# Optimization experiments

Measured on AMD Instinct MI355X. Metric: run time of the kernel, lower is better.

Reference implementation:

```python
import jax, jax.numpy as jnp
import numpy as np

B, D = 256, 8                 # trees, tree depth (leaves at level D)
V, E, H = 32000, 128, 128     # vocab, embedding_dim, hidden_dim
N = 2 ** (D + 1) - 1          # 511 heap-indexed nodes per tree


def setup_inputs() -> dict:
    key = jax.random.key(0)
    ks = jax.random.split(key, 9)
    s = 0.05  # keep gate pre-activations in a sane range
    return {
        "tokens": jax.random.randint(ks[0], (B, N), 0, V),
        "arity": jax.random.randint(ks[1], (B, 2 ** D - 1), 0, 2).astype(jnp.int32),
        "emb": jax.random.normal(ks[2], (V, E), dtype=jnp.float32) * s,
        "W": jax.random.normal(ks[3], (4, E, H), dtype=jnp.float32) * s,      # i,f,o,u
        "bW": jax.random.normal(ks[4], (4, H), dtype=jnp.float32) * s,
        "Ubin": jax.random.normal(ks[5], (5, 2 * H, H), dtype=jnp.float32) * s,  # i,f_l,f_r,o,u
        "bUbin": jax.random.normal(ks[6], (5, H), dtype=jnp.float32) * s,
        "Uun": jax.random.normal(ks[7], (4, H, H), dtype=jnp.float32) * s,    # i,f,o,u
        "bUun": jax.random.normal(ks[8], (4, H), dtype=jnp.float32) * s,
    }


def reference(tokens, arity, emb, W, bW, Ubin, bUbin, Uun, bUun):
    # Level-synchronous bottom-up Tree-LSTM over heap-indexed perfect trees.
    x = emb[tokens]  # [B, N, E] embedding gather for every node
    depth = int(np.log2(tokens.shape[1] + 1)) - 1

    # Leaves (level `depth`): h = tanh(W_u x + b_u), c = 0
    off = 2 ** depth - 1
    lx = x[:, off:]  # [B, 2^D, E]
    h = jnp.tanh(jnp.einsum('bne,eh->bnh', lx, W[3]) + bW[3])
    c = jnp.zeros_like(h)

    for l in range(depth - 1, -1, -1):
        o2, cnt = 2 ** l - 1, 2 ** l
        nx = x[:, o2:o2 + cnt]            # [B, cnt, E] this level's tokens
        h_l, h_r = h[:, ::2], h[:, 1::2]   # children (heap order)
        c_l, c_r = c[:, ::2], c[:, 1::2]

        # Shared input projections for all 4 gates, fused into one GEMM
        Wx = jnp.einsum('bne,geh->gbnh', nx, W) + bW[:, None, None, :]
        hcat = jnp.concatenate([h_l, h_r], axis=-1)  # [B, cnt, 2H]
        Ub = jnp.einsum('bnk,gkh->gbnh', hcat, Ubin) + bUbin[:, None, None, :]
        Uu = jnp.einsum('bnh,gha->gbna', h_l, Uun) + bUun[:, None, None, :]

        # Binary branch: i, f_l, f_r (shared W_f), o, u
        i_b = jax.nn.sigmoid(Wx[0] + Ub[0])
        f_lg = jax.nn.sigmoid(Wx[1] + Ub[1])
        f_rg = jax.nn.sigmoid(Wx[1] + Ub[2])
        o_b = jax.nn.sigmoid(Wx[2] + Ub[3])
        u_b = jnp.tanh(Wx[3] + Ub[4])
        c_b = i_b * u_b + f_lg * c_l + f_rg * c_r
        h_b = o_b * jnp.tanh(c_b)

        # Unary branch (child = left child)
        i_u = jax.nn.sigmoid(Wx[0] + Uu[0])
        f_u = jax.nn.sigmoid(Wx[1] + Uu[1])
        o_u = jax.nn.sigmoid(Wx[2] + Uu[2])
        u_u = jnp.tanh(Wx[3] + Uu[3])
        c_u = i_u * u_u + f_u * c_l
        h_u = o_u * jnp.tanh(c_u)

        m = (arity[:, o2:o2 + cnt] == 1)[..., None]  # True -> binary node
        h = jnp.where(m, h_b, h_u)
        c = jnp.where(m, c_b, c_u)

    return h[:, 0], c[:, 0]  # root (h, c), each [B, H]
```

## Files before the change

### kernel.cpp

```cpp
#include <hip/hip_runtime.h>
#include <hip/hip_bf16.h>

#define NTOK 511
#define NINT 255

typedef unsigned short u16;
typedef __attribute__((ext_vector_type(8))) short bf16x8;
typedef __attribute__((ext_vector_type(4))) float f32x4;

constexpr int OFF_FLAG = 0;
constexpr int OFF_WB   = 4;
constexpr int W3B = 294912;
constexpr int WB_ELEMS = 311296;
constexpr int OFF_BIAS = OFF_WB + WB_ELEMS / 2;
constexpr int BW4 = 0, BUB4 = 512, BUB1 = 1024, BUU4 = 1152, B3 = 1664;
constexpr int BIAS_FLOATS = 1792;
constexpr int OFF_ROOT  = OFF_BIAS + BIAS_FLOATS;
constexpr int OFF_CHUNK = OFF_ROOT + 65536;
constexpr long PER_TREE = 49152;

__device__ __forceinline__ float bf2f(__hip_bfloat16 v) { return __bfloat162float(v); }
__device__ __forceinline__ short f2s(float f) {
    __hip_bfloat16 b = __float2bfloat16(f);
    return *reinterpret_cast<short*>(&b);
}
__device__ __forceinline__ float sigm(float x) { return 1.0f / (1.0f + __expf(-x)); }
__device__ __forceinline__ float tanh_(float x) { return 1.0f - 2.0f / (__expf(2.0f * x) + 1.0f); }

__device__ __forceinline__ float ldf(const void* p, long idx, int isbf) {
    return isbf ? bf2f(((const __hip_bfloat16*)p)[idx]) : ((const float*)p)[idx];
}

__device__ __forceinline__ bf16x8 ldA(const void* p, long idx, int isbf) {
    if (isbf) return *(const bf16x8*)((const short*)p + idx);
    const float* f = (const float*)p + idx;
    float4 a = *(const float4*)f, b = *(const float4*)(f + 4);
    bf16x8 r;
    r[0] = f2s(a.x); r[1] = f2s(a.y); r[2] = f2s(a.z); r[3] = f2s(a.w);
    r[4] = f2s(b.x); r[5] = f2s(b.y); r[6] = f2s(b.z); r[7] = f2s(b.w);
    return r;
}

typedef const __attribute__((address_space(1))) unsigned int* gp1_t;
typedef __attribute__((address_space(3))) unsigned int* lp3_t;
__device__ __forceinline__ void stage16(const void* g, void* l) {
    __builtin_amdgcn_global_load_lds((gp1_t)g, (lp3_t)l, 16, 0, 0);
}

__global__ void detect_kernel(const void* W, float* ws) {
    if (threadIdx.x == 0 && blockIdx.x == 0) {
        const u16* u = (const u16*)W;
        int cnt = 0;
        for (int i = 0; i < 128; i += 2) {
            u16 x = u[i];
            int ex = (x >> 7) & 0xff;
            if (x == 0 || (ex >= 96 && ex <= 127)) cnt++;
        }
        ((int*)ws)[0] = (cnt >= 48) ? 1 : 0;
    }
}

__global__ __launch_bounds__(256) void repack_mfma(
    const void* W, const void* bW, const void* Ubin, const void* bUbin,
    const void* Uun, const void* bUun, float* ws)
{
    const int isbf = ((const int*)ws)[0];
    short* wb = (short*)(ws + OFF_WB);
    float* bias = ws + OFF_BIAS;
    int tid = blockIdx.x * blockDim.x + threadIdx.x;
    int nth = gridDim.x * blockDim.x;

    for (int idx = tid; idx < 294912; idx += nth) {
        int e = idx & 511, fjc = idx >> 9;
        int jc = fjc / 72, f = fjc - jc * 72;
        int lane = e >> 3, id8 = e & 7;
        int j = jc * 16 + (lane & 15);
        float v;
        if (f < 16) {
            int g = f >> 2, ks = f & 3;
            int k = ks * 32 + (lane >> 4) * 8 + id8;
            v = ldf(W, (long)g * 16384 + k * 128 + j, isbf);
        } else if (f < 32) {
            int fu = f - 16; int g = fu >> 2, ks = fu & 3;
            int k = ks * 32 + (lane >> 4) * 8 + id8;
            v = ldf(Uun, (long)g * 16384 + k * 128 + j, isbf);
        } else {
            int fb = f - 32; int g = fb >> 3, ks = fb & 7;
            int k = ks * 32 + (lane >> 4) * 8 + id8;
            v = ldf(Ubin, (long)g * 32768 + k * 128 + j, isbf);
        }
        wb[idx] = f2s(v);
    }
    for (int idx = tid; idx < 16384; idx += nth) {
        int e = idx & 511, frag = idx >> 9;
        int jc = frag >> 2, ks = frag & 3;
        int lane = e >> 3, id8 = e & 7;
        int k = ks * 32 + (lane >> 4) * 8 + id8;
        int j = jc * 16 + (lane & 15);
        wb[W3B + idx] = f2s(ldf(W, (long)3 * 16384 + k * 128 + j, isbf));
    }
    for (int j = tid; j < 128; j += nth) {
        float4 b;
        b.x = ldf(bW, 0 * 128 + j, isbf); b.y = ldf(bW, 1 * 128 + j, isbf);
        b.z = ldf(bW, 2 * 128 + j, isbf); b.w = ldf(bW, 3 * 128 + j, isbf);
        ((float4*)(bias + BW4))[j] = b;
        float4 bb;
        bb.x = ldf(bUbin, 0 * 128 + j, isbf); bb.y = ldf(bUbin, 1 * 128 + j, isbf);
        bb.z = ldf(bUbin, 2 * 128 + j, isbf); bb.w = ldf(bUbin, 3 * 128 + j, isbf);
        ((float4*)(bias + BUB4))[j] = bb;
        (bias + BUB1)[j] = ldf(bUbin, 4 * 128 + j, isbf);
        float4 bu;
        bu.x = ldf(bUun, 0 * 128 + j, isbf); bu.y = ldf(bUun, 1 * 128 + j, isbf);
        bu.z = ldf(bUun, 2 * 128 + j, isbf); bu.w = ldf(bUun, 3 * 128 + j, isbf);
        ((float4*)(bias + BUU4))[j] = bu;
        (bias + B3)[j] = ldf(bW, 3 * 128 + j, isbf);
    }
}

#define MFMA(A, B, C) __builtin_amdgcn_mfma_f32_16x16x32_bf16(A, B, C, 0, 0, 0)

__global__ __launch_bounds__(256, 2) void leaf_mfma(
    const int* __restrict__ tokens, const void* emb, const float* __restrict__ ws,
    short* __restrict__ hOut, int treeOff, int Mtot, int iters)
{
    __shared__ short hst[4][16][132];
    const int t = threadIdx.x;
    const int isbf = ((const int*)ws)[0];
    const int wv = t >> 6, lane = t & 63, quad = lane >> 4, l16 = lane & 15;
    const short* wb = (const short*)(ws + OFF_WB);
    const float* bias = ws + OFF_BIAS;

    bf16x8 bf[32];
#pragma unroll
    for (int f = 0; f < 32; ++f)
        bf[f] = *(const bf16x8*)(wb + W3B + f * 512 + lane * 8);
    float b3v[8];
#pragma unroll
    for (int jc = 0; jc < 8; ++jc) b3v[jc] = (bias + B3)[jc * 16 + l16];

    for (int it = 0; it < iters; ++it) {
        int rb = (blockIdx.x * iters + it) * 64 + wv * 16;
        if (rb >= Mtot) break;
        int p = rb + l16; if (p >= Mtot) p = Mtot - 1;
        int bl = p >> 8, i = p & 255;
        int tk = tokens[(long)(treeOff + bl) * NTOK + 255 + i];
        bf16x8 ax[4];
#pragma unroll
        for (int ks = 0; ks < 4; ++ks)
            ax[ks] = ldA(emb, (long)tk * 128 + ks * 32 + quad * 8, isbf);
        f32x4 acc[8];
#pragma unroll
        for (int jc = 0; jc < 8; ++jc) acc[jc] = {0.f, 0.f, 0.f, 0.f};
#pragma unroll
        for (int jc = 0; jc < 8; ++jc)
#pragma unroll
            for (int ks = 0; ks < 4; ++ks)
                acc[jc] = MFMA(ax[ks], bf[jc * 4 + ks], acc[jc]);
#pragma unroll
        for (int jc = 0; jc < 8; ++jc)
#pragma unroll
            for (int r = 0; r < 4; ++r)
                hst[wv][quad * 4 + r][jc * 16 + l16] = f2s(tanh_(acc[jc][r] + b3v[jc]));
        int nloc = lane >> 2, c0 = (lane & 3) * 4;
        int prow = rb + nloc;
        if (prow < Mtot) {
#pragma unroll
            for (int jcb = 0; jcb < 8; ++jcb) {
                uint2 v = *(const uint2*)&hst[wv][nloc][jcb * 16 + c0];
                *(uint2*)&hOut[((long)jcb * Mtot + prow) * 16 + c0] = v;
            }
        }
    }
}

__global__ __launch_bounds__(256, 2) void level2_mfma(
    const int* __restrict__ tokens, const int* __restrict__ arity, const void* emb,
    const float* __restrict__ ws, const short* __restrict__ hChild,
    const float* __restrict__ cChild, short* __restrict__ hOut, float* __restrict__ cOut,
    int lvl, int treeOff, int leafchild, int Mtot, int Mchild,
    int NBMB, int Q)
{
    __shared__ short Bs[72 * 512];
    __shared__ short hst[4][16][20];

    const int t = threadIdx.x;
    const int isbf = ((const int*)ws)[0];
    const int jc = blockIdx.x / NBMB;
    const int mb = blockIdx.x - jc * NBMB;
    const int wv = t >> 6, lane = t & 63, quad = lane >> 4, l16 = lane & 15;
    const int cnt = 1 << lvl, o2 = cnt - 1;
    const short* wb = (const short*)(ws + OFF_WB);
    const float* bias = ws + OFF_BIAS;
    const short* wj = wb + (long)jc * 36864;

#pragma unroll
    for (int s = 0; s < 18; ++s) {
        int off = (s * 256 + t) * 8;
        stage16(wj + off, Bs + off);
    }

    const int j = jc * 16 + l16;
    const float4 bw = ((const float4*)(bias + BW4))[j];
    const float4 bb = ((const float4*)(bias + BUB4))[j];
    const float  b1 = (bias + BUB1)[j];
    const float4 bu = ((const float4*)(bias + BUU4))[j];

    __syncthreads();

    for (int q = 0; q < Q; ++q) {
        const int p0 = (mb * Q + q) * 64;
        if (p0 >= Mtot) break;

        int row = wv * 16 + l16;
        int p = p0 + row; if (p >= Mtot) p = Mtot - 1;
        int bl = p >> lvl, i = p - (bl << lvl);
        long crow = (long)bl * (cnt << 1) + 2 * i;
        int tk = tokens[(long)(treeOff + bl) * NTOK + o2 + i];
        bf16x8 ax[4], ah[8];
#pragma unroll
        for (int ks = 0; ks < 4; ++ks)
            ax[ks] = ldA(emb, (long)tk * 128 + ks * 32 + quad * 8, isbf);
#pragma unroll
        for (int ks = 0; ks < 8; ++ks) {
            int k0 = ks * 32 + quad * 8;
            int side = k0 >> 7, kl = k0 & 127;
            ah[ks] = *(const bf16x8*)(hChild +
                ((long)(kl >> 4) * Mchild + crow + side) * 16 + (kl & 15));
        }

        f32x4 aW[4], aU[4], aB[5];
#pragma unroll
        for (int g = 0; g < 4; ++g) { aW[g] = {0,0,0,0}; aU[g] = {0,0,0,0}; }
#pragma unroll
        for (int g = 0; g < 5; ++g) aB[g] = {0,0,0,0};

#pragma unroll
        for (int f = 0; f < 16; ++f) {
            bf16x8 b = *(const bf16x8*)&Bs[f * 512 + lane * 8];
            aW[f >> 2] = MFMA(ax[f & 3], b, aW[f >> 2]);
        }
#pragma unroll
        for (int f = 16; f < 32; ++f) {
            bf16x8 b = *(const bf16x8*)&Bs[f * 512 + lane * 8];
            aU[(f - 16) >> 2] = MFMA(ah[(f - 16) & 3], b, aU[(f - 16) >> 2]);
        }
#pragma unroll
        for (int f = 32; f < 72; ++f) {
            bf16x8 b = *(const bf16x8*)&Bs[f * 512 + lane * 8];
            int fb = f - 32;
            aB[fb >> 3] = MFMA(ah[fb & 7], b, aB[fb >> 3]);
        }

        int arv[4]; float clv[4], crv[4];
#pragma unroll
        for (int r = 0; r < 4; ++r) {
            int pe = p0 + wv * 16 + quad * 4 + r;
            if (pe >= Mtot) pe = Mtot - 1;
            int ble = pe >> lvl, ie = pe - (ble << lvl);
            arv[r] = arity[(long)(treeOff + ble) * NINT + o2 + ie];
            if (!leafchild) {
                long crowe = (long)ble * (cnt << 1) + 2 * ie;
                clv[r] = cChild[((long)jc * Mchild + crowe) * 16 + l16];
                crv[r] = cChild[((long)jc * Mchild + crowe + 1) * 16 + l16];
            } else { clv[r] = 0.f; crv[r] = 0.f; }
        }

#pragma unroll
        for (int r = 0; r < 4; ++r) {
            int ml = wv * 16 + quad * 4 + r;
            int pr = p0 + ml;
            bool val = (pr < Mtot);
            int pc = val ? pr : Mtot - 1;
            bool bin = (arv[r] == 1);
            float w0 = aW[0][r] + bw.x;
            float w1 = aW[1][r] + bw.y;
            float w2 = aW[2][r] + bw.z;
            float w3 = aW[3][r] + bw.w;
            float pi, pf, po, pu;
            if (bin) { pi = w0 + aB[0][r] + bb.x; pf = w1 + aB[1][r] + bb.y;
                       po = w2 + aB[3][r] + bb.w; pu = w3 + aB[4][r] + b1; }
            else     { pi = w0 + aU[0][r] + bu.x; pf = w1 + aU[1][r] + bu.y;
                       po = w2 + aU[2][r] + bu.z; pu = w3 + aU[3][r] + bu.w; }
            float cl = clv[r];
            float cr = bin ? crv[r] : 0.f;
            float frv = bin ? sigm(w1 + aB[2][r] + bb.z) : 0.f;
            float ig = sigm(pi), fg = sigm(pf), og = sigm(po), ug = tanh_(pu);
            float c = ig * ug + fg * cl + frv * cr;
            float h = og * tanh_(c);
            if (val) cOut[((long)jc * Mtot + pc) * 16 + l16] = c;
            hst[wv][quad * 4 + r][l16] = f2s(h);
        }
        {
            int nloc = lane >> 2, c0 = (lane & 3) * 4;
            int prow = p0 + wv * 16 + nloc;
            if (prow < Mtot) {
                uint2 v = *(const uint2*)&hst[wv][nloc][c0];
                *(uint2*)&hOut[((long)jc * Mtot + prow) * 16 + c0] = v;
            }
        }
    }
}

__global__ __launch_bounds__(256, 2) void level_direct(
    const int* __restrict__ tokens, const int* __restrict__ arity, const void* emb,
    const float* __restrict__ ws, const short* __restrict__ hChild,
    const float* __restrict__ cChild, short* __restrict__ hOut, float* __restrict__ cOut,
    float* __restrict__ rootH, float* __restrict__ rootC,
    int lvl, int treeOff, int isRoot, int Mtot, int Mchild, int NBM)
{
    __shared__ short hst[4][16][20];

    const int t = threadIdx.x;
    const int isbf = ((const int*)ws)[0];
    const int jc = blockIdx.x / NBM;
    const int mb = blockIdx.x - jc * NBM;
    const int wv = t >> 6, lane = t & 63, quad = lane >> 4, l16 = lane & 15;
    const int cnt = 1 << lvl, o2 = cnt - 1;
    const short* wb = (const short*)(ws + OFF_WB);
    const float* bias = ws + OFF_BIAS;
    const short* wj = wb + (long)jc * 36864;

    const int j = jc * 16 + l16;
    const float4 bw = ((const float4*)(bias + BW4))[j];
    const float4 bb = ((const float4*)(bias + BUB4))[j];
    const float  b1 = (bias + BUB1)[j];
    const float4 bu = ((const float4*)(bias + BUU4))[j];

    const int p0 = mb * 64;

    int row = wv * 16 + l16;
    int p = p0 + row; if (p >= Mtot) p = Mtot - 1;
    int bl = p >> lvl, i = p - (bl << lvl);
    long crow = (long)bl * (cnt << 1) + 2 * i;
    int tk = tokens[(long)(treeOff + bl) * NTOK + o2 + i];
    bf16x8 ax[4], ah[8];
#pragma unroll
    for (int ks = 0; ks < 4; ++ks)
        ax[ks] = ldA(emb, (long)tk * 128 + ks * 32 + quad * 8, isbf);
#pragma unroll
    for (int ks = 0; ks < 8; ++ks) {
        int k0 = ks * 32 + quad * 8;
        int side = k0 >> 7, kl = k0 & 127;
        ah[ks] = *(const bf16x8*)(hChild +
            ((long)(kl >> 4) * Mchild + crow + side) * 16 + (kl & 15));
    }

    f32x4 aW[4], aU[4], aB[5];
#pragma unroll
    for (int g = 0; g < 4; ++g) { aW[g] = {0,0,0,0}; aU[g] = {0,0,0,0}; }
#pragma unroll
    for (int g = 0; g < 5; ++g) aB[g] = {0,0,0,0};

#pragma unroll
    for (int f = 0; f < 16; ++f) {
        bf16x8 b = *(const bf16x8*)(wj + f * 512 + lane * 8);
        aW[f >> 2] = MFMA(ax[f & 3], b, aW[f >> 2]);
    }
#pragma unroll
    for (int f = 16; f < 32; ++f) {
        bf16x8 b = *(const bf16x8*)(wj + f * 512 + lane * 8);
        aU[(f - 16) >> 2] = MFMA(ah[(f - 16) & 3], b, aU[(f - 16) >> 2]);
    }
#pragma unroll
    for (int f = 32; f < 72; ++f) {
        bf16x8 b = *(const bf16x8*)(wj + f * 512 + lane * 8);
        int fb = f - 32;
        aB[fb >> 3] = MFMA(ah[fb & 7], b, aB[fb >> 3]);
    }

    int arv[4]; float clv[4], crv[4];
#pragma unroll
    for (int r = 0; r < 4; ++r) {
        int pe = p0 + wv * 16 + quad * 4 + r;
        if (pe >= Mtot) pe = Mtot - 1;
        int ble = pe >> lvl, ie = pe - (ble << lvl);
        arv[r] = arity[(long)(treeOff + ble) * NINT + o2 + ie];
        long crowe = (long)ble * (cnt << 1) + 2 * ie;
        clv[r] = cChild[((long)jc * Mchild + crowe) * 16 + l16];
        crv[r] = cChild[((long)jc * Mchild + crowe + 1) * 16 + l16];
    }

#pragma unroll
    for (int r = 0; r < 4; ++r) {
        int ml = wv * 16 + quad * 4 + r;
        int pr = p0 + ml;
        bool val = (pr < Mtot);
        int pc = val ? pr : Mtot - 1;
        int ble = pc >> lvl;
        bool bin = (arv[r] == 1);
        float w0 = aW[0][r] + bw.x;
        float w1 = aW[1][r] + bw.y;
        float w2 = aW[2][r] + bw.z;
        float w3 = aW[3][r] + bw.w;
        float pi, pf, po, pu;
        if (bin) { pi = w0 + aB[0][r] + bb.x; pf = w1 + aB[1][r] + bb.y;
                   po = w2 + aB[3][r] + bb.w; pu = w3 + aB[4][r] + b1; }
        else     { pi = w0 + aU[0][r] + bu.x; pf = w1 + aU[1][r] + bu.y;
                   po = w2 + aU[2][r] + bu.z; pu = w3 + aU[3][r] + bu.w; }
        float cl = clv[r];
        float cr = bin ? crv[r] : 0.f;
        float frv = bin ? sigm(w1 + aB[2][r] + bb.z) : 0.f;
        float ig = sigm(pi), fg = sigm(pf), og = sigm(po), ug = tanh_(pu);
        float c = ig * ug + fg * cl + frv * cr;
        float h = og * tanh_(c);
        if (isRoot) {
            if (val) {
                rootH[(long)(treeOff + ble) * 128 + j] = h;
                rootC[(long)(treeOff + ble) * 128 + j] = c;
            }
        } else {
            if (val) cOut[((long)jc * Mtot + pc) * 16 + l16] = c;
            hst[wv][quad * 4 + r][l16] = f2s(h);
        }
    }
    if (!isRoot) {
        int nloc = lane >> 2, c0 = (lane & 3) * 4;
        int prow = p0 + wv * 16 + nloc;
        if (prow < Mtot) {
            uint2 v = *(const uint2*)&hst[wv][nloc][c0];
            *(uint2*)&hOut[((long)jc * Mtot + prow) * 16 + c0] = v;
        }
    }
}

__global__ __launch_bounds__(256) void out_kernel(const float* ws, void* out)
{
    const int isbf = ((const int*)ws)[0];
    const float* rootH = ws + OFF_ROOT;
    const float* rootC = rootH + 32768;
    int t = blockIdx.x * 256 + threadIdx.x;
    float h = rootH[t], c = rootC[t];
    if (isbf) {
        ((__hip_bfloat16*)out)[t]         = __float2bfloat16(h);
        ((__hip_bfloat16*)out)[32768 + t] = __float2bfloat16(c);
    } else {
        ((float*)out)[t]         = h;
        ((float*)out)[32768 + t] = c;
    }
}

extern "C" void kernel_launch(void* const* d_in, const int* in_sizes, int n_in,
                              void* d_out, int out_size, void* d_ws, size_t ws_size,
                              hipStream_t stream)
{
    const int* tokens = (const int*)d_in[0];
    const int* arity  = (const int*)d_in[1];
    const void* emb   = d_in[2];
    const void* W     = d_in[3];
    const void* bW    = d_in[4];
    const void* Ubin  = d_in[5];
    const void* bUbin = d_in[6];
    const void* Uun   = d_in[7];
    const void* bUun  = d_in[8];

    float* ws = (float*)d_ws;

    int Bc = 256;
    while (Bc > 1 && (size_t)(OFF_CHUNK + Bc * PER_TREE) * 4 > ws_size) Bc >>= 1;
    const int nCh = 256 / Bc;

    detect_kernel<<<1, 64, 0, stream>>>(W, ws);
    repack_mfma<<<128, 256, 0, stream>>>(W, bW, Ubin, bUbin, Uun, bUun, ws);

    short* Ha = (short*)(ws + OFF_CHUNK);
    short* Hb = Ha + (long)Bc * 32768;
    float* Ca = (float*)(Hb + (long)Bc * 16384);
    float* Cb = Ca + (long)Bc * 8192;
    float* rootH = ws + OFF_ROOT;
    float* rootC = rootH + 32768;

    for (int cidx = 0; cidx < nCh; ++cidx) {
        int toff = cidx * Bc;
        {
            int Mleaf = Bc * 256;
            int NBL = (Mleaf + 63) / 64; if (NBL > 512) NBL = 512;
            int itersL = (Mleaf + NBL * 64 - 1) / (NBL * 64);
            leaf_mfma<<<NBL, 256, 0, stream>>>(tokens, emb, ws, Ha, toff, Mleaf, itersL);
        }
        for (int l = 7; l >= 5; --l) {
            int M = Bc << l;
            int Mchild = Bc << (l + 1);
            const short* hC = (l & 1) ? Ha : Hb;
            const float* cC = (l & 1) ? Ca : Cb;
            short* hO = (l & 1) ? Hb : Ha;
            float* cO = (l & 1) ? Cb : Ca;
            int lc = (l == 7) ? 1 : 0;
            int NBM = (M + 63) / 64;
            int Q = (NBM + 127) / 128;
            int NBMB = (NBM + Q - 1) / Q;
            level2_mfma<<<dim3(NBMB * 8), 256, 0, stream>>>(
                tokens, arity, emb, ws, hC, cC, hO, cO,
                l, toff, lc, M, Mchild, NBMB, Q);
        }
        for (int l = 4; l >= 0; --l) {
            int M = Bc << l;
            int Mchild = Bc << (l + 1);
            const short* hC = (l & 1) ? Ha : Hb;
            const float* cC = (l & 1) ? Ca : Cb;
            short* hO = (l & 1) ? Hb : Ha;
            float* cO = (l & 1) ? Cb : Ca;
            int isRoot = (l == 0) ? 1 : 0;
            int NBM = (M + 63) / 64;
            level_direct<<<dim3(NBM * 8), 256, 0, stream>>>(
                tokens, arity, emb, ws, hC, cC, hO, cO, rootH, rootC,
                l, toff, isRoot, M, Mchild, NBM);
        }
    }
    out_kernel<<<128, 256, 0, stream>>>(ws, d_out);
}
```

Before: 184.4 us.

## Process two M-tiles per wave in level2_mfma to reuse LDS weight fragments

level2_mfma becomes a template over MT row tiles per wave, so each B fragment read from LDS feeds MT MFMAs. The host now launches MT=2 with 128 nodes per block and half the grid. The child c-state loads are hoisted ahead of the MFMA chain and the arity loads moved into the epilogue, in both level2_mfma and level_direct, to overlap memory latency with compute. This raises register pressure (double the accumulators and A fragments) and halves block-level parallelism.

Measured after the change: 182.5 us. About the same (-1.0%).

```diff
diff --git a/kernel.cpp b/kernel.cpp
--- a/kernel.cpp
+++ b/kernel.cpp
@@ -173,6 +173,7 @@
     }
 }
 
+template <int MT>
 __global__ __launch_bounds__(256, 2) void level2_mfma(
     const int* __restrict__ tokens, const int* __restrict__ arity, const void* emb,
     const float* __restrict__ ws, const short* __restrict__ hChild,
@@ -181,8 +182,9 @@
     int NBMB, int Q)
 {
     __shared__ short Bs[72 * 512];
-    __shared__ short hst[4][16][20];
-
+    __shared__ short hst[4][MT][16][20];
+
+    constexpr int NODES = 64 * MT;
     const int t = threadIdx.x;
     const int isbf = ((const int*)ws)[0];
     const int jc = blockIdx.x / NBMB;
@@ -208,94 +210,117 @@
     __syncthreads();
 
     for (int q = 0; q < Q; ++q) {
-        const int p0 = (mb * Q + q) * 64;
+        const int p0 = (mb * Q + q) * NODES;
         if (p0 >= Mtot) break;
 
-        int row = wv * 16 + l16;
-        int p = p0 + row; if (p >= Mtot) p = Mtot - 1;
-        int bl = p >> lvl, i = p - (bl << lvl);
-        long crow = (long)bl * (cnt << 1) + 2 * i;
-        int tk = tokens[(long)(treeOff + bl) * NTOK + o2 + i];
-        bf16x8 ax[4], ah[8];
-#pragma unroll
-        for (int ks = 0; ks < 4; ++ks)
-            ax[ks] = ldA(emb, (long)tk * 128 + ks * 32 + quad * 8, isbf);
-#pragma unroll
-        for (int ks = 0; ks < 8; ++ks) {
-            int k0 = ks * 32 + quad * 8;
-            int side = k0 >> 7, kl = k0 & 127;
-            ah[ks] = *(const bf16x8*)(hChild +
-                ((long)(kl >> 4) * Mchild + crow + side) * 16 + (kl & 15));
-        }
-
-        f32x4 aW[4], aU[4], aB[5];
-#pragma unroll
-        for (int g = 0; g < 4; ++g) { aW[g] = {0,0,0,0}; aU[g] = {0,0,0,0}; }
-#pragma unroll
-        for (int g = 0; g < 5; ++g) aB[g] = {0,0,0,0};
+        bf16x8 ax[MT][4], ah[MT][8];
+#pragma unroll
+        for (int mt = 0; mt < MT; ++mt) {
+            int row = wv * (16 * MT) + mt * 16 + l16;
+            int p = p0 + row; if (p >= Mtot) p = Mtot - 1;
+            int bl = p >> lvl, i = p - (bl << lvl);
+            long crow = (long)bl * (cnt << 1) + 2 * i;
+            int tk = tokens[(long)(treeOff + bl) * NTOK + o2 + i];
+#pragma unroll
+            for (int ks = 0; ks < 4; ++ks)
+                ax[mt][ks] = ldA(emb, (long)tk * 128 + ks * 32 + quad * 8, isbf);
+#pragma unroll
+            for (int ks = 0; ks < 8; ++ks) {
+                int k0 = ks * 32 + quad * 8;
+                int side = k0 >> 7, kl = k0 & 127;
+                ah[mt][ks] = *(const bf16x8*)(hChild +
+                    ((long)(kl >> 4) * Mchild + crow + side) * 16 + (kl & 15));
+            }
+        }
+
+        float clv[MT][4], crv[MT][4];
+#pragma unroll
+        for (int mt = 0; mt < MT; ++mt)
+#pragma unroll
+        for (int r = 0; r < 4; ++r) {
+            if (!leafchild) {
+                int pe = p0 + wv * (16 * MT) + mt * 16 + quad * 4 + r;
+                if (pe >= Mtot) pe = Mtot - 1;
+                int ble = pe >> lvl, ie = pe - (ble << lvl);
+                long crowe = (long)ble * (cnt << 1) + 2 * ie;
+                clv[mt][r] = cChild[((long)jc * Mchild + crowe) * 16 + l16];
+                crv[mt][r] = cChild[((long)jc * Mchild + crowe + 1) * 16 + l16];
+            } else { clv[mt][r] = 0.f; crv[mt][r] = 0.f; }
+        }
+
+        f32x4 aW[4][MT], aU[4][MT], aB[5][MT];
+#pragma unroll
+        for (int g = 0; g < 4; ++g)
+#pragma unroll
+            for (int mt = 0; mt < MT; ++mt) { aW[g][mt] = {0,0,0,0}; aU[g][mt] = {0,0,0,0}; }
+#pragma unroll
+        for (int g = 0; g < 5; ++g)
+#pragma unroll
+            for (int mt = 0; mt < MT; ++mt) aB[g][mt] = {0,0,0,0};
 
 #pragma unroll
         for (int f = 0; f < 16; ++f) {
             bf16x8 b = *(const bf16x8*)&Bs[f * 512 + lane * 8];
-            aW[f >> 2] = MFMA(ax[f & 3], b, aW[f >> 2]);
+#pragma unroll
+            for (int mt = 0; mt < MT; ++mt)
+                aW[f >> 2][mt] = MFMA(ax[mt][f & 3], b, aW[f >> 2][mt]);
         }
 #pragma unroll
         for (int f = 16; f < 32; ++f) {
             bf16x8 b = *(const bf16x8*)&Bs[f * 512 + lane * 8];
-            aU[(f - 16) >> 2] = MFMA(ah[(f - 16) & 3], b, aU[(f - 16) >> 2]);
+            int g = (f - 16) >> 2, ks = (f - 16) & 3;
+#pragma unroll
+            for (int mt = 0; mt < MT; ++mt)
+                aU[g][mt] = MFMA(ah[mt][ks], b, aU[g][mt]);
         }
 #pragma unroll
         for (int f = 32; f < 72; ++f) {
             bf16x8 b = *(const bf16x8*)&Bs[f * 512 + lane * 8];
-            int fb = f - 32;
-            aB[fb >> 3] = MFMA(ah[fb & 7], b, aB[fb >> 3]);
-        }
-
-        int arv[4]; float clv[4], crv[4];
-#pragma unroll
-        for (int r = 0; r < 4; ++r) {
-            int pe = p0 + wv * 16 + quad * 4 + r;
-            if (pe >= Mtot) pe = Mtot - 1;
-            int ble = pe >> lvl, ie = pe - (ble << lvl);
-            arv[r] = arity[(long)(treeOff + ble) * NINT + o2 + ie];
-            if (!leafchild) {
-                long crowe = (long)ble * (cnt << 1) + 2 * ie;
-                clv[r] = cChild[((long)jc * Mchild + crowe) * 16 + l16];
-                crv[r] = cChild[((long)jc * Mchild + crowe + 1) * 16 + l16];
-            } else { clv[r] = 0.f; crv[r] = 0.f; }
-        }
-
-#pragma unroll
-        for (int r = 0; r < 4; ++r) {
-            int ml = wv * 16 + quad * 4 + r;
-            int pr = p0 + ml;
-            bool val = (pr < Mtot);
-            int pc = val ? pr : Mtot - 1;
-            bool bin = (arv[r] == 1);
-            float w0 = aW[0][r] + bw.x;
-            float w1 = aW[1][r] + bw.y;
-            float w2 = aW[2][r] + bw.z;
-            float w3 = aW[3][r] + bw.w;
-            float pi, pf, po, pu;
-            if (bin) { pi = w0 + aB[0][r] + bb.x; pf = w1 + aB[1][r] + bb.y;
-                       po = w2 + aB[3][r] + bb.w; pu = w3 + aB[4][r] + b1; }
-            else     { pi = w0 + aU[0][r] + bu.x; pf = w1 + aU[1][r] + bu.y;
-                       po = w2 + aU[2][r] + bu.z; pu = w3 + aU[3][r] + bu.w; }
-            float cl = clv[r];
-            float cr = bin ? crv[r] : 0.f;
-            float frv = bin ? sigm(w1 + aB[2][r] + bb.z) : 0.f;
-            float ig = sigm(pi), fg = sigm(pf), og = sigm(po), ug = tanh_(pu);
-            float c = ig * ug + fg * cl + frv * cr;
-            float h = og * tanh_(c);
-            if (val) cOut[((long)jc * Mtot + pc) * 16 + l16] = c;
-            hst[wv][quad * 4 + r][l16] = f2s(h);
+            int fb = f - 32, g = fb >> 3, ks = fb & 7;
+#pragma unroll
+            for (int mt = 0; mt < MT; ++mt)
+                aB[g][mt] = MFMA(ah[mt][ks], b, aB[g][mt]);
+        }
+
+#pragma unroll
+        for (int mt = 0; mt < MT; ++mt) {
+#pragma unroll
+            for (int r = 0; r < 4; ++r) {
+                int ml = wv * (16 * MT) + mt * 16 + quad * 4 + r;
+                int pr = p0 + ml;
+                bool val = (pr < Mtot);
+                int pc = val ? pr : Mtot - 1;
+                int ble = pc >> lvl, ie = pc - (ble << lvl);
+                int arvv = arity[(long)(treeOff + ble) * NINT + o2 + ie];
+                bool bin = (arvv == 1);
+                float w0 = aW[0][mt][r] + bw.x;
+                float w1 = aW[1][mt][r] + bw.y;
+                float w2 = aW[2][mt][r] + bw.z;
+                float w3 = aW[3][mt][r] + bw.w;
+                float pi, pf, po, pu;
+                if (bin) { pi = w0 + aB[0][mt][r] + bb.x; pf = w1 + aB[1][mt][r] + bb.y;
+                           po = w2 + aB[3][mt][r] + bb.w; pu = w3 + aB[4][mt][r] + b1; }
+                else     { pi = w0 + aU[0][mt][r] + bu.x; pf = w1 + aU[1][mt][r] + bu.y;
+                           po = w2 + aU[2][mt][r] + bu.z; pu = w3 + aU[3][mt][r] + bu.w; }
+                float cl = clv[mt][r];
+                float cr = bin ? crv[mt][r] : 0.f;
+                float frv = bin ? sigm(w1 + aB[2][mt][r] + bb.z) : 0.f;
+                float ig = sigm(pi), fg = sigm(pf), og = sigm(po), ug = tanh_(pu);
+                float c = ig * ug + fg * cl + frv * cr;
+                float h = og * tanh_(c);
+                if (val) cOut[((long)jc * Mtot + pc) * 16 + l16] = c;
+                hst[wv][mt][quad * 4 + r][l16] = f2s(h);
+            }
         }
         {
             int nloc = lane >> 2, c0 = (lane & 3) * 4;
-            int prow = p0 + wv * 16 + nloc;
-            if (prow < Mtot) {
-                uint2 v = *(const uint2*)&hst[wv][nloc][c0];
-                *(uint2*)&hOut[((long)jc * Mtot + prow) * 16 + c0] = v;
+#pragma unroll
+            for (int mt = 0; mt < MT; ++mt) {
+                int prow = p0 + wv * (16 * MT) + mt * 16 + nloc;
+                if (prow < Mtot) {
+                    uint2 v = *(const uint2*)&hst[wv][mt][nloc][c0];
+                    *(uint2*)&hOut[((long)jc * Mtot + prow) * 16 + c0] = v;
+                }
             }
         }
     }
@@ -345,6 +370,17 @@
             ((long)(kl >> 4) * Mchild + crow + side) * 16 + (kl & 15));
     }
 
+    float clv[4], crv[4];
+#pragma unroll
+    for (int r = 0; r < 4; ++r) {
+        int pe = p0 + wv * 16 + quad * 4 + r;
+        if (pe >= Mtot) pe = Mtot - 1;
+        int ble = pe >> lvl, ie = pe - (ble << lvl);
+        long crowe = (long)ble * (cnt << 1) + 2 * ie;
+        clv[r] = cChild[((long)jc * Mchild + crowe) * 16 + l16];
+        crv[r] = cChild[((long)jc * Mchild + crowe + 1) * 16 + l16];
+    }
+
     f32x4 aW[4], aU[4], aB[5];
 #pragma unroll
     for (int g = 0; g < 4; ++g) { aW[g] = {0,0,0,0}; aU[g] = {0,0,0,0}; }
@@ -366,18 +402,6 @@
         bf16x8 b = *(const bf16x8*)(wj + f * 512 + lane * 8);
         int fb = f - 32;
         aB[fb >> 3] = MFMA(ah[fb & 7], b, aB[fb >> 3]);
-    }
-
-    int arv[4]; float clv[4], crv[4];
-#pragma unroll
-    for (int r = 0; r < 4; ++r) {
-        int pe = p0 + wv * 16 + quad * 4 + r;
-        if (pe >= Mtot) pe = Mtot - 1;
-        int ble = pe >> lvl, ie = pe - (ble << lvl);
-        arv[r] = arity[(long)(treeOff + ble) * NINT + o2 + ie];
-        long crowe = (long)ble * (cnt << 1) + 2 * ie;
-        clv[r] = cChild[((long)jc * Mchild + crowe) * 16 + l16];
-        crv[r] = cChild[((long)jc * Mchild + crowe + 1) * 16 + l16];
     }
 
 #pragma unroll
@@ -386,8 +410,9 @@
         int pr = p0 + ml;
         bool val = (pr < Mtot);
         int pc = val ? pr : Mtot - 1;
-        int ble = pc >> lvl;
-        bool bin = (arv[r] == 1);
+        int ble = pc >> lvl, ie = pc - (ble << lvl);
+        int arvv = arity[(long)(treeOff + ble) * NINT + o2 + ie];
+        bool bin = (arvv == 1);
         float w0 = aW[0][r] + bw.x;
         float w1 = aW[1][r] + bw.y;
         float w2 = aW[2][r] + bw.z;
@@ -485,10 +510,10 @@
             short* hO = (l & 1) ? Hb : Ha;
             float* cO = (l & 1) ? Cb : Ca;
             int lc = (l == 7) ? 1 : 0;
-            int NBM = (M + 63) / 64;
-            int Q = (NBM + 127) / 128;
+            int NBM = (M + 127) / 128;
+            int Q = (NBM + 63) / 64;
             int NBMB = (NBM + Q - 1) / Q;
-            level2_mfma<<<dim3(NBMB * 8), 256, 0, stream>>>(
+            level2_mfma<2><<<dim3(NBMB * 8), 256, 0, stream>>>(
                 tokens, arity, emb, ws, hC, cC, hO, cO,
                 l, toff, lc, M, Mchild, NBMB, Q);
         }
```

## Unify level kernels into one direct-load kernel with grouped block swizzle

Applied to the files above, without the earlier changes.

Replaces the LDS-staged level2_mfma kernel (used for levels 7..5) and level_direct with a single level_all kernel. It reads weight fragments straight from global memory instead of staging 72 KB into shared memory, and raises the occupancy hint to 3 blocks per SM. When NBM is a multiple of 8, it remaps block IDs so neighbouring blocks share row tiles across the 8 column chunks, which should improve L2 reuse of activations. The aim is to cut LDS staging and the per-block sync and to run more blocks at once, at the cost of heavier global/L2 traffic for weights and losing the multi-tile Q loop that amortised staging.

New measurement: 233.5 us. +26.6%, slower.

```diff
diff --git a/kernel.cpp b/kernel.cpp
--- a/kernel.cpp
+++ b/kernel.cpp
@@ -39,12 +39,6 @@
     r[0] = f2s(a.x); r[1] = f2s(a.y); r[2] = f2s(a.z); r[3] = f2s(a.w);
     r[4] = f2s(b.x); r[5] = f2s(b.y); r[6] = f2s(b.z); r[7] = f2s(b.w);
     return r;
-}
-
-typedef const __attribute__((address_space(1))) unsigned int* gp1_t;
-typedef __attribute__((address_space(3))) unsigned int* lp3_t;
-__device__ __forceinline__ void stage16(const void* g, void* l) {
-    __builtin_amdgcn_global_load_lds((gp1_t)g, (lp3_t)l, 16, 0, 0);
 }
 
 __global__ void detect_kernel(const void* W, float* ws) {
@@ -173,159 +167,33 @@
     }
 }
 
-__global__ __launch_bounds__(256, 2) void level2_mfma(
+__global__ __launch_bounds__(256, 3) void level_all(
     const int* __restrict__ tokens, const int* __restrict__ arity, const void* emb,
     const float* __restrict__ ws, const short* __restrict__ hChild,
     const float* __restrict__ cChild, short* __restrict__ hOut, float* __restrict__ cOut,
-    int lvl, int treeOff, int leafchild, int Mtot, int Mchild,
-    int NBMB, int Q)
-{
-    __shared__ short Bs[72 * 512];
+    float* __restrict__ rootH, float* __restrict__ rootC,
+    int lvl, int treeOff, int leafchild, int isRoot, int Mtot, int Mchild, int NBM)
+{
     __shared__ short hst[4][16][20];
 
     const int t = threadIdx.x;
     const int isbf = ((const int*)ws)[0];
-    const int jc = blockIdx.x / NBMB;
-    const int mb = blockIdx.x - jc * NBMB;
+    int jc, mb;
+    {
+        int bid = blockIdx.x;
+        if ((NBM & 7) == 0) {
+            int g = bid >> 6, r = bid & 63;
+            jc = r >> 3; mb = g * 8 + (r & 7);
+        } else {
+            jc = bid / NBM; mb = bid - jc * NBM;
+        }
+    }
     const int wv = t >> 6, lane = t & 63, quad = lane >> 4, l16 = lane & 15;
     const int cnt = 1 << lvl, o2 = cnt - 1;
     const short* wb = (const short*)(ws + OFF_WB);
     const float* bias = ws + OFF_BIAS;
     const short* wj = wb + (long)jc * 36864;
-
-#pragma unroll
-    for (int s = 0; s < 18; ++s) {
-        int off = (s * 256 + t) * 8;
-        stage16(wj + off, Bs + off);
-    }
-
     const int j = jc * 16 + l16;
-    const float4 bw = ((const float4*)(bias + BW4))[j];
-    const float4 bb = ((const float4*)(bias + BUB4))[j];
-    const float  b1 = (bias + BUB1)[j];
-    const float4 bu = ((const float4*)(bias + BUU4))[j];
-
-    __syncthreads();
-
-    for (int q = 0; q < Q; ++q) {
-        const int p0 = (mb * Q + q) * 64;
-        if (p0 >= Mtot) break;
-
-        int row = wv * 16 + l16;
-        int p = p0 + row; if (p >= Mtot) p = Mtot - 1;
-        int bl = p >> lvl, i = p - (bl << lvl);
-        long crow = (long)bl * (cnt << 1) + 2 * i;
-        int tk = tokens[(long)(treeOff + bl) * NTOK + o2 + i];
-        bf16x8 ax[4], ah[8];
-#pragma unroll
-        for (int ks = 0; ks < 4; ++ks)
-            ax[ks] = ldA(emb, (long)tk * 128 + ks * 32 + quad * 8, isbf);
-#pragma unroll
-        for (int ks = 0; ks < 8; ++ks) {
-            int k0 = ks * 32 + quad * 8;
-            int side = k0 >> 7, kl = k0 & 127;
-            ah[ks] = *(const bf16x8*)(hChild +
-                ((long)(kl >> 4) * Mchild + crow + side) * 16 + (kl & 15));
-        }
-
-        f32x4 aW[4], aU[4], aB[5];
-#pragma unroll
-        for (int g = 0; g < 4; ++g) { aW[g] = {0,0,0,0}; aU[g] = {0,0,0,0}; }
-#pragma unroll
-        for (int g = 0; g < 5; ++g) aB[g] = {0,0,0,0};
-
-#pragma unroll
-        for (int f = 0; f < 16; ++f) {
-            bf16x8 b = *(const bf16x8*)&Bs[f * 512 + lane * 8];
-            aW[f >> 2] = MFMA(ax[f & 3], b, aW[f >> 2]);
-        }
-#pragma unroll
-        for (int f = 16; f < 32; ++f) {
-            bf16x8 b = *(const bf16x8*)&Bs[f * 512 + lane * 8];
-            aU[(f - 16) >> 2] = MFMA(ah[(f - 16) & 3], b, aU[(f - 16) >> 2]);
-        }
-#pragma unroll
-        for (int f = 32; f < 72; ++f) {
-            bf16x8 b = *(const bf16x8*)&Bs[f * 512 + lane * 8];
-            int fb = f - 32;
-            aB[fb >> 3] = MFMA(ah[fb & 7], b, aB[fb >> 3]);
-        }
-
-        int arv[4]; float clv[4], crv[4];
-#pragma unroll
-        for (int r = 0; r < 4; ++r) {
-            int pe = p0 + wv * 16 + quad * 4 + r;
-            if (pe >= Mtot) pe = Mtot - 1;
-            int ble = pe >> lvl, ie = pe - (ble << lvl);
-            arv[r] = arity[(long)(treeOff + ble) * NINT + o2 + ie];
-            if (!leafchild) {
-                long crowe = (long)ble * (cnt << 1) + 2 * ie;
-                clv[r] = cChild[((long)jc * Mchild + crowe) * 16 + l16];
-                crv[r] = cChild[((long)jc * Mchild + crowe + 1) * 16 + l16];
-            } else { clv[r] = 0.f; crv[r] = 0.f; }
-        }
-
-#pragma unroll
-        for (int r = 0; r < 4; ++r) {
-            int ml = wv * 16 + quad * 4 + r;
-            int pr = p0 + ml;
-            bool val = (pr < Mtot);
-            int pc = val ? pr : Mtot - 1;
-            bool bin = (arv[r] == 1);
-            float w0 = aW[0][r] + bw.x;
-            float w1 = aW[1][r] + bw.y;
-            float w2 = aW[2][r] + bw.z;
-            float w3 = aW[3][r] + bw.w;
-            float pi, pf, po, pu;
-            if (bin) { pi = w0 + aB[0][r] + bb.x; pf = w1 + aB[1][r] + bb.y;
-                       po = w2 + aB[3][r] + bb.w; pu = w3 + aB[4][r] + b1; }
-            else     { pi = w0 + aU[0][r] + bu.x; pf = w1 + aU[1][r] + bu.y;
-                       po = w2 + aU[2][r] + bu.z; pu = w3 + aU[3][r] + bu.w; }
-            float cl = clv[r];
-            float cr = bin ? crv[r] : 0.f;
-            float frv = bin ? sigm(w1 + aB[2][r] + bb.z) : 0.f;
-            float ig = sigm(pi), fg = sigm(pf), og = sigm(po), ug = tanh_(pu);
-            float c = ig * ug + fg * cl + frv * cr;
-            float h = og * tanh_(c);
-            if (val) cOut[((long)jc * Mtot + pc) * 16 + l16] = c;
-            hst[wv][quad * 4 + r][l16] = f2s(h);
-        }
-        {
-            int nloc = lane >> 2, c0 = (lane & 3) * 4;
-            int prow = p0 + wv * 16 + nloc;
-            if (prow < Mtot) {
-                uint2 v = *(const uint2*)&hst[wv][nloc][c0];
-                *(uint2*)&hOut[((long)jc * Mtot + prow) * 16 + c0] = v;
-            }
-        }
-    }
-}
-
-__global__ __launch_bounds__(256, 2) void level_direct(
-    const int* __restrict__ tokens, const int* __restrict__ arity, const void* emb,
-    const float* __restrict__ ws, const short* __restrict__ hChild,
-    const float* __restrict__ cChild, short* __restrict__ hOut, float* __restrict__ cOut,
-    float* __restrict__ rootH, float* __restrict__ rootC,
-    int lvl, int treeOff, int isRoot, int Mtot, int Mchild, int NBM)
-{
-    __shared__ short hst[4][16][20];
-
-    const int t = threadIdx.x;
-    const int isbf = ((const int*)ws)[0];
-    const int jc = blockIdx.x / NBM;
-    const int mb = blockIdx.x - jc * NBM;
-    const int wv = t >> 6, lane = t & 63, quad = lane >> 4, l16 = lane & 15;
-    const int cnt = 1 << lvl, o2 = cnt - 1;
-    const short* wb = (const short*)(ws + OFF_WB);
-    const float* bias = ws + OFF_BIAS;
-    const short* wj = wb + (long)jc * 36864;
-
-    const int j = jc * 16 + l16;
-    const float4 bw = ((const float4*)(bias + BW4))[j];
-    const float4 bb = ((const float4*)(bias + BUB4))[j];
-    const float  b1 = (bias + BUB1)[j];
-    const float4 bu = ((const float4*)(bias + BUU4))[j];
-
     const int p0 = mb * 64;
 
     int row = wv * 16 + l16;
@@ -345,29 +213,6 @@
             ((long)(kl >> 4) * Mchild + crow + side) * 16 + (kl & 15));
     }
 
-    f32x4 aW[4], aU[4], aB[5];
-#pragma unroll
-    for (int g = 0; g < 4; ++g) { aW[g] = {0,0,0,0}; aU[g] = {0,0,0,0}; }
-#pragma unroll
-    for (int g = 0; g < 5; ++g) aB[g] = {0,0,0,0};
-
-#pragma unroll
-    for (int f = 0; f < 16; ++f) {
-        bf16x8 b = *(const bf16x8*)(wj + f * 512 + lane * 8);
-        aW[f >> 2] = MFMA(ax[f & 3], b, aW[f >> 2]);
-    }
-#pragma unroll
-    for (int f = 16; f < 32; ++f) {
-        bf16x8 b = *(const bf16x8*)(wj + f * 512 + lane * 8);
-        aU[(f - 16) >> 2] = MFMA(ah[(f - 16) & 3], b, aU[(f - 16) >> 2]);
-    }
-#pragma unroll
-    for (int f = 32; f < 72; ++f) {
-        bf16x8 b = *(const bf16x8*)(wj + f * 512 + lane * 8);
-        int fb = f - 32;
-        aB[fb >> 3] = MFMA(ah[fb & 7], b, aB[fb >> 3]);
-    }
-
     int arv[4]; float clv[4], crv[4];
 #pragma unroll
     for (int r = 0; r < 4; ++r) {
@@ -375,10 +220,40 @@
         if (pe >= Mtot) pe = Mtot - 1;
         int ble = pe >> lvl, ie = pe - (ble << lvl);
         arv[r] = arity[(long)(treeOff + ble) * NINT + o2 + ie];
-        long crowe = (long)ble * (cnt << 1) + 2 * ie;
-        clv[r] = cChild[((long)jc * Mchild + crowe) * 16 + l16];
-        crv[r] = cChild[((long)jc * Mchild + crowe + 1) * 16 + l16];
-    }
+        if (!leafchild) {
+            long crowe = (long)ble * (cnt << 1) + 2 * ie;
+            clv[r] = cChild[((long)jc * Mchild + crowe) * 16 + l16];
+            crv[r] = cChild[((long)jc * Mchild + crowe + 1) * 16 + l16];
+        } else { clv[r] = 0.f; crv[r] = 0.f; }
+    }
+
+    f32x4 aW[4], aU[4], aB[5];
+#pragma unroll
+    for (int g = 0; g < 4; ++g) { aW[g] = {0,0,0,0}; aU[g] = {0,0,0,0}; }
+#pragma unroll
+    for (int g = 0; g < 5; ++g) aB[g] = {0,0,0,0};
+
+#pragma unroll
+    for (int f = 0; f < 16; ++f) {
+        bf16x8 b = *(const bf16x8*)(wj + f * 512 + lane * 8);
+        aW[f >> 2] = MFMA(ax[f & 3], b, aW[f >> 2]);
+    }
+#pragma unroll
+    for (int f = 16; f < 32; ++f) {
+        bf16x8 b = *(const bf16x8*)(wj + f * 512 + lane * 8);
+        aU[(f - 16) >> 2] = MFMA(ah[(f - 16) & 3], b, aU[(f - 16) >> 2]);
+    }
+#pragma unroll
+    for (int f = 32; f < 72; ++f) {
+        bf16x8 b = *(const bf16x8*)(wj + f * 512 + lane * 8);
+        int fb = f - 32;
+        aB[fb >> 3] = MFMA(ah[fb & 7], b, aB[fb >> 3]);
+    }
+
+    const float4 bw = ((const float4*)(bias + BW4))[j];
+    const float4 bb = ((const float4*)(bias + BUB4))[j];
+    const float  b1 = (bias + BUB1)[j];
+    const float4 bu = ((const float4*)(bias + BUU4))[j];
 
 #pragma unroll
     for (int r = 0; r < 4; ++r) {
@@ -477,7 +352,7 @@
             int itersL = (Mleaf + NBL * 64 - 1) / (NBL * 64);
             leaf_mfma<<<NBL, 256, 0, stream>>>(tokens, emb, ws, Ha, toff, Mleaf, itersL);
         }
-        for (int l = 7; l >= 5; --l) {
+        for (int l = 7; l >= 0; --l) {
             int M = Bc << l;
             int Mchild = Bc << (l + 1);
             const short* hC = (l & 1) ? Ha : Hb;
@@ -485,25 +360,11 @@
             short* hO = (l & 1) ? Hb : Ha;
             float* cO = (l & 1) ? Cb : Ca;
             int lc = (l == 7) ? 1 : 0;
-            int NBM = (M + 63) / 64;
-            int Q = (NBM + 127) / 128;
-            int NBMB = (NBM + Q - 1) / Q;
-            level2_mfma<<<dim3(NBMB * 8), 256, 0, stream>>>(
-                tokens, arity, emb, ws, hC, cC, hO, cO,
-                l, toff, lc, M, Mchild, NBMB, Q);
-        }
-        for (int l = 4; l >= 0; --l) {
-            int M = Bc << l;
-            int Mchild = Bc << (l + 1);
-            const short* hC = (l & 1) ? Ha : Hb;
-            const float* cC = (l & 1) ? Ca : Cb;
-            short* hO = (l & 1) ? Hb : Ha;
-            float* cO = (l & 1) ? Cb : Ca;
             int isRoot = (l == 0) ? 1 : 0;
             int NBM = (M + 63) / 64;
-            level_direct<<<dim3(NBM * 8), 256, 0, stream>>>(
+            level_all<<<dim3(NBM * 8), 256, 0, stream>>>(
                 tokens, arity, emb, ws, hC, cC, hO, cO, rootH, rootC,
-                l, toff, isRoot, M, Mchild, NBM);
+                l, toff, lc, isRoot, M, Mchild, NBM);
         }
     }
     out_kernel<<<128, 256, 0, stream>>>(ws, d_out);
```
